# Kernel tuning notes

Hardware: AMD Instinct MI355X
Metric: run time of the kernel (lower is better)

The kernel has to match this reference:

```python
import jax, jax.numpy as jnp
import numpy as np
from jax import lax

NUM_INITS = 64
MODEL_MODE = ['conv', 'conv', 'dense']
SIZE_ARRAY = [(16, 1, 5, 5), (16,), (32, 16, 5, 5), (32,), (10, 512), (10,)]
_flat = [int(np.prod(s)) for s in SIZE_ARRAY]
BP = np.concatenate(([0], np.cumsum(_flat)))  # breakpoints into flat param vector
TOTAL_PARAMS = int(BP[-1])  # 18378
BATCH_N = 128


def setup_inputs() -> dict:
    key = jax.random.key(0)
    k1, k2 = jax.random.split(key)
    params = jax.random.normal(k1, (NUM_INITS, TOTAL_PARAMS), dtype=jnp.float32) * 0.05
    batch = jax.random.normal(k2, (BATCH_N, 1, 28, 28), dtype=jnp.float32)
    return {"params": params, "batch": batch}


def _conv_relu_pool(x, w, b):
    # x: (N, C_in, H, W), w: (C_out, C_in, k, k), b: (C_out,)
    y = lax.conv_general_dilated(x, w, window_strides=(1, 1), padding='VALID',
                                 dimension_numbers=('NCHW', 'OIHW', 'NCHW'))
    y = jax.nn.relu(y + b[None, :, None, None])
    # MaxPool2d(2, 2) over spatial dims
    return lax.reduce_window(y, -jnp.inf, lax.max, (1, 1, 2, 2), (1, 1, 2, 2), 'VALID')


def reference(params, batch):
    # out: (num_inits, N, C, H, W) — ensemble replicated batch
    out = jnp.broadcast_to(batch[None], (NUM_INITS,) + batch.shape)
    i = 0
    for mode in MODEL_MODE:
        w = params[:, BP[i]:BP[i + 1]].reshape((NUM_INITS,) + SIZE_ARRAY[i])
        b = params[:, BP[i + 1]:BP[i + 2]].reshape((NUM_INITS,) + SIZE_ARRAY[i + 1])
        if mode == 'conv':
            # grouped conv over inits == vmap of dense conv over the init axis
            out = jax.vmap(_conv_relu_pool)(out, w, b)
        else:  # dense
            out = out.reshape(out.shape[0], out.shape[1], -1)  # flatten C,H,W
            out = jnp.einsum('inf,iof->ino', out, w) + b[:, None, :]
        i += 2
    return jax.nn.log_softmax(out, axis=2)  # (num_inits, N, 10)
```

## Files before the change

### kernel.cpp

```cpp
#include <hip/hip_runtime.h>
#include <hip/hip_bf16.h>
#include <math.h>

#define P_TOTAL 18378

typedef __attribute__((ext_vector_type(8))) short short8;
typedef __attribute__((ext_vector_type(4))) float float4v;
typedef __attribute__((ext_vector_type(16))) float float16;

__device__ __forceinline__ unsigned short f2bf(float f) {
    union { float f; unsigned u; } v; v.f = f;
    unsigned r = v.u + 0x7fffu + ((v.u >> 16) & 1u);
    return (unsigned short)(r >> 16);
}
__device__ __forceinline__ float bf2f(unsigned short h) {
    union { unsigned u; float f; } v; v.u = ((unsigned)h) << 16;
    return v.f;
}

__global__ __launch_bounds__(256) void prep_kernel(
        const float* __restrict__ params,
        const float* __restrict__ batch,
        unsigned short* __restrict__ wswz,
        float* __restrict__ w3lf,
        unsigned short* __restrict__ w1bf,
        unsigned short* __restrict__ Bmat) {
    int blk = blockIdx.x;
    int t = threadIdx.x;
    if (blk < 64) {
        int i = blk;
        const float* w2 = params + (size_t)i * P_TOTAL + 416;
        unsigned short* dst = wswz + (size_t)i * 12800;
        for (int k = t; k < 12800; k += 256) {
            int co = k / 400;
            int r = k - co * 400;
            int cin = r / 25;
            int s = r - cin * 25;
            dst[(s * 32 + co) * 16 + cin] = f2bf(w2[k]);
        }
        const float* w3 = params + (size_t)i * P_TOTAL + 13248;
        float* d3 = w3lf + (size_t)i * 5120;
        for (int k = t; k < 5120; k += 256) {
            int o = k >> 9, r = k & 511;
            int l = r >> 3, s = r & 7;
            int co = l & 31, h = l >> 5;
            int py = s >> 1, d = s & 1;
            d3[k] = w3[o * 512 + co * 16 + py * 4 + 2 * h + d];
        }
        const float* w1 = params + (size_t)i * P_TOTAL;
        unsigned short* d1 = w1bf + (size_t)i * 512;
        for (int e = t; e < 512; e += 256) {
            int m = e >> 5, k = e & 31;
            d1[e] = (k < 25) ? f2bf(w1[m * 25 + k]) : (unsigned short)0;
        }
    } else {
        __shared__ float img[784];
        int j = blk - 64;
        const float* ip = batch + j * 784;
        for (int k = t; k < 784; k += 256) img[k] = ip[k];
        __syncthreads();
        unsigned short* dst = Bmat + (size_t)j * 18432;
        for (int task = t; task < 2304; task += 256) {
            int c = task >> 2, kh = task & 3;
            int pp = c >> 2, q = c & 3;
            int py = pp / 12, px = pp - py * 12;
            int y0 = 2 * py + (q >> 1);
            int x0 = 2 * px + (q & 1);
            unsigned short ov[8] __attribute__((aligned(16)));
#pragma unroll
            for (int u = 0; u < 8; ++u) {
                int k = kh * 8 + u;
                float v = 0.f;
                if (k < 25) {
                    int ky = k / 5, kx = k - ky * 5;
                    v = img[(y0 + ky) * 28 + x0 + kx];
                }
                ov[u] = f2bf(v);
            }
            *(uint4*)(dst + c * 32 + kh * 8) = *(const uint4*)ov;
        }
    }
}

#define A1_PIX_STRIDE 24
#define IMG_LDS (144 * A1_PIX_STRIDE)
__global__ __launch_bounds__(256, 5) void mega_kernel(
        const float* __restrict__ params,
        const unsigned short* __restrict__ Bmat,
        const unsigned short* __restrict__ w1bf,
        const unsigned short* __restrict__ wswz,
        const float* __restrict__ w3lf,
        float* __restrict__ out) {
    __shared__ unsigned short a1s[4 * IMG_LDS];
    int b = blockIdx.x;
    int i = b & 63;
    int g = b >> 6;
    int t = threadIdx.x;
    int w = t >> 6;
    int lane = t & 63;
    int j = g * 4 + w;

    {
        int co = lane & 15;
        int h4 = lane >> 4;
        short8 wfr = *(const short8*)(w1bf + (size_t)i * 512 + co * 32 + h4 * 8);
        float bias1 = params[(size_t)i * P_TOTAL + 400 + co];
        unsigned short* dst = a1s + w * IMG_LDS;
        const unsigned short* bsrc = Bmat + (size_t)j * 18432;
#pragma unroll 6
        for (int nt = 0; nt < 36; ++nt) {
            short8 afr = *(const short8*)(bsrc + (nt * 16 + co) * 32 + h4 * 8);
            float4v acc = {0.f, 0.f, 0.f, 0.f};
            acc = __builtin_amdgcn_mfma_f32_16x16x32_bf16(afr, wfr, acc, 0, 0, 0);
            float v = fmaxf(fmaxf(acc[0], acc[1]), fmaxf(acc[2], acc[3]));
            v = fmaxf(v + bias1, 0.f);
            dst[(nt * 4 + h4) * A1_PIX_STRIDE + co] = f2bf(v);
        }
    }

    int n = lane & 31;
    int h = lane >> 5;
    const short8* wg = (const short8*)(wswz + (size_t)i * 12800 + n * 16 + h * 8);
    int y0 = n >> 3, x0 = n & 7;
    const unsigned short* bbase = a1s + w * IMG_LDS;
    const short8* pptr0 = (const short8*)(bbase + ((y0    ) * 12 + x0) * A1_PIX_STRIDE + h * 8);
    const short8* pptr1 = (const short8*)(bbase + ((y0 + 4) * 12 + x0) * A1_PIX_STRIDE + h * 8);

    float16 acc0 = {};
    float16 acc1 = {};
#pragma unroll
    for (int ky = 0; ky < 5; ++ky) {
#pragma unroll
        for (int kx = 0; kx < 5; ++kx) {
            int tap = ky * 5 + kx;
            short8 wf = wg[tap * 64];
            int bo = (ky * 12 + kx) * 3;
            short8 p0 = pptr0[bo];
            short8 p1 = pptr1[bo];
            acc0 = __builtin_amdgcn_mfma_f32_32x32x16_bf16(p0, wf, acc0, 0, 0, 0);
            acc1 = __builtin_amdgcn_mfma_f32_32x32x16_bf16(p1, wf, acc1, 0, 0, 0);
        }
    }

    int co2 = lane & 31;
    float bias2 = params[(size_t)i * P_TOTAL + 13216 + co2];
    float xr[8];
#pragma unroll
    for (int pyl = 0; pyl < 2; ++pyl) {
#pragma unroll
        for (int d = 0; d < 2; ++d) {
            int base = pyl * 8 + d * 2;
            float v0 = fmaxf(fmaxf(acc0[base], acc0[base + 1]),
                             fmaxf(acc0[base + 4], acc0[base + 5]));
            float v1 = fmaxf(fmaxf(acc1[base], acc1[base + 1]),
                             fmaxf(acc1[base + 4], acc1[base + 5]));
            xr[pyl * 2 + d]     = fmaxf(v0 + bias2, 0.f);
            xr[4 + pyl * 2 + d] = fmaxf(v1 + bias2, 0.f);
        }
    }

    const float* w3p = w3lf + (size_t)i * 5120 + lane * 8;
    float acc[10];
#pragma unroll
    for (int o = 0; o < 10; ++o) {
        float4v u0 = *(const float4v*)(w3p + o * 512);
        float4v u1 = *(const float4v*)(w3p + o * 512 + 4);
        float a = 0.f;
        a = fmaf(xr[0], u0[0], a);
        a = fmaf(xr[1], u0[1], a);
        a = fmaf(xr[2], u0[2], a);
        a = fmaf(xr[3], u0[3], a);
        a = fmaf(xr[4], u1[0], a);
        a = fmaf(xr[5], u1[1], a);
        a = fmaf(xr[6], u1[2], a);
        a = fmaf(xr[7], u1[3], a);
#pragma unroll
        for (int d = 32; d >= 1; d >>= 1) a += __shfl_xor(a, d, 64);
        acc[o] = a;
    }
    const float* bp = params + (size_t)i * P_TOTAL + 18368;
    float m = -3.4e38f;
#pragma unroll
    for (int o = 0; o < 10; ++o) { acc[o] += bp[o]; m = fmaxf(m, acc[o]); }
    float ssum = 0.f;
#pragma unroll
    for (int o = 0; o < 10; ++o) ssum += __expf(acc[o] - m);
    float ls = __logf(ssum) + m;
    if (lane == 0) {
        float* op = out + ((size_t)i * 128 + j) * 10;
#pragma unroll
        for (int o = 0; o < 10; ++o) op[o] = acc[o] - ls;
    }
}

extern "C" void kernel_launch(void* const* d_in, const int* in_sizes, int n_in,
                              void* d_out, int out_size, void* d_ws, size_t ws_size,
                              hipStream_t stream) {
    const float* params = (const float*)d_in[0];
    const float* batch  = (const float*)d_in[1];
    float* out = (float*)d_out;

    unsigned short* wswz = (unsigned short*)d_ws;
    float* w3lf = (float*)((char*)d_ws + 1638400);
    unsigned short* w1bf = (unsigned short*)((char*)d_ws + 1638400 + 1310720);
    unsigned short* Bmat = (unsigned short*)((char*)d_ws + 1638400 + 1310720 + 65536);

    prep_kernel<<<192, 256, 0, stream>>>(params, batch, wswz, w3lf, w1bf, Bmat);
    mega_kernel<<<2048, 256, 0, stream>>>(params, Bmat, w1bf, wswz, w3lf, out);
}
```

Before: 105.5 us.

## Split prep work across more blocks, use DPP reductions, hardware bf16 convert, setprio

The prep kernel now splits each init's weight reformatting across 8 blocks and each image's im2col across 2 blocks, giving 768 blocks instead of 192 so more of the GPU is used during the prep phase. In the main kernel, the 64-lane shuffle-xor reduction becomes a DPP row/bcast sequence that leaves the total in lane 63, and only that lane computes the log-softmax. The float-to-bf16 conversion now uses the v_cvt_pk_bf16_f32 instruction, and s_setprio raises wave priority around the MFMA loop. The DPP broadcast steps depend on exact lane semantics, so a wrong control code would give wrong sums.

```diff
diff --git a/kernel.cpp b/kernel.cpp
--- a/kernel.cpp
+++ b/kernel.cpp
@@ -9,13 +9,23 @@
 typedef __attribute__((ext_vector_type(16))) float float16;
 
 __device__ __forceinline__ unsigned short f2bf(float f) {
-    union { float f; unsigned u; } v; v.f = f;
-    unsigned r = v.u + 0x7fffu + ((v.u >> 16) & 1u);
-    return (unsigned short)(r >> 16);
-}
-__device__ __forceinline__ float bf2f(unsigned short h) {
-    union { unsigned u; float f; } v; v.u = ((unsigned)h) << 16;
-    return v.f;
+    unsigned r;
+    asm("v_cvt_pk_bf16_f32 %0, %1, %1" : "=v"(r) : "v"(f));
+    return (unsigned short)r;
+}
+
+#define DPP_ADD_STEP(x, ctrl)                                                  \
+    x += __int_as_float(__builtin_amdgcn_update_dpp(                           \
+            0, __float_as_int(x), ctrl, 0xf, 0xf, true))
+
+__device__ __forceinline__ float wave_reduce_sum63(float x) {
+    DPP_ADD_STEP(x, 0x111);
+    DPP_ADD_STEP(x, 0x112);
+    DPP_ADD_STEP(x, 0x114);
+    DPP_ADD_STEP(x, 0x118);
+    DPP_ADD_STEP(x, 0x142);
+    DPP_ADD_STEP(x, 0x143);
+    return x;
 }
 
 __global__ __launch_bounds__(256) void prep_kernel(
@@ -27,40 +37,45 @@
         unsigned short* __restrict__ Bmat) {
     int blk = blockIdx.x;
     int t = threadIdx.x;
-    if (blk < 64) {
-        int i = blk;
-        const float* w2 = params + (size_t)i * P_TOTAL + 416;
-        unsigned short* dst = wswz + (size_t)i * 12800;
-        for (int k = t; k < 12800; k += 256) {
-            int co = k / 400;
-            int r = k - co * 400;
-            int cin = r / 25;
-            int s = r - cin * 25;
-            dst[(s * 32 + co) * 16 + cin] = f2bf(w2[k]);
-        }
-        const float* w3 = params + (size_t)i * P_TOTAL + 13248;
-        float* d3 = w3lf + (size_t)i * 5120;
-        for (int k = t; k < 5120; k += 256) {
-            int o = k >> 9, r = k & 511;
-            int l = r >> 3, s = r & 7;
-            int co = l & 31, h = l >> 5;
-            int py = s >> 1, d = s & 1;
-            d3[k] = w3[o * 512 + co * 16 + py * 4 + 2 * h + d];
-        }
-        const float* w1 = params + (size_t)i * P_TOTAL;
-        unsigned short* d1 = w1bf + (size_t)i * 512;
-        for (int e = t; e < 512; e += 256) {
-            int m = e >> 5, k = e & 31;
-            d1[e] = (k < 25) ? f2bf(w1[m * 25 + k]) : (unsigned short)0;
+    if (blk < 512) {
+        int i = blk >> 3;
+        int p = blk & 7;
+        const float* P = params + (size_t)i * P_TOTAL;
+        int s0 = p * 2304;
+        for (int s = s0 + t; s < s0 + 2304; s += 256) {
+            if (s < 12800) {
+                int co = s / 400;
+                int r = s - co * 400;
+                int cin = r / 25;
+                int sk = r - cin * 25;
+                wswz[(size_t)i * 12800 + (sk * 32 + co) * 16 + cin] =
+                    f2bf(P[416 + s]);
+            } else if (s < 17920) {
+                int k = s - 12800;
+                int o = k >> 9, r = k & 511;
+                int l = r >> 3, sl = r & 7;
+                int co = l & 31, h = l >> 5;
+                int py = sl >> 1, d = sl & 1;
+                w3lf[(size_t)i * 5120 + k] =
+                    P[13248 + o * 512 + co * 16 + py * 4 + 2 * h + d];
+            } else {
+                int e = s - 17920;
+                int m = e >> 5, k = e & 31;
+                w1bf[(size_t)i * 512 + e] =
+                    (k < 25) ? f2bf(P[m * 25 + k]) : (unsigned short)0;
+            }
         }
     } else {
         __shared__ float img[784];
-        int j = blk - 64;
+        int jb = blk - 512;
+        int j = jb >> 1;
+        int half = jb & 1;
         const float* ip = batch + j * 784;
         for (int k = t; k < 784; k += 256) img[k] = ip[k];
         __syncthreads();
         unsigned short* dst = Bmat + (size_t)j * 18432;
-        for (int task = t; task < 2304; task += 256) {
+        int task0 = half * 1152;
+        for (int task = task0 + t; task < task0 + 1152; task += 256) {
             int c = task >> 2, kh = task & 3;
             int pp = c >> 2, q = c & 3;
             int py = pp / 12, px = pp - py * 12;
@@ -128,6 +143,7 @@
 
     float16 acc0 = {};
     float16 acc1 = {};
+    __builtin_amdgcn_s_setprio(1);
 #pragma unroll
     for (int ky = 0; ky < 5; ++ky) {
 #pragma unroll
@@ -141,6 +157,7 @@
             acc1 = __builtin_amdgcn_mfma_f32_32x32x16_bf16(p1, wf, acc1, 0, 0, 0);
         }
     }
+    __builtin_amdgcn_s_setprio(0);
 
     int co2 = lane & 31;
     float bias2 = params[(size_t)i * P_TOTAL + 13216 + co2];
@@ -174,19 +191,17 @@
         a = fmaf(xr[5], u1[1], a);
         a = fmaf(xr[6], u1[2], a);
         a = fmaf(xr[7], u1[3], a);
-#pragma unroll
-        for (int d = 32; d >= 1; d >>= 1) a += __shfl_xor(a, d, 64);
-        acc[o] = a;
-    }
-    const float* bp = params + (size_t)i * P_TOTAL + 18368;
-    float m = -3.4e38f;
-#pragma unroll
-    for (int o = 0; o < 10; ++o) { acc[o] += bp[o]; m = fmaxf(m, acc[o]); }
-    float ssum = 0.f;
-#pragma unroll
-    for (int o = 0; o < 10; ++o) ssum += __expf(acc[o] - m);
-    float ls = __logf(ssum) + m;
-    if (lane == 0) {
+        acc[o] = wave_reduce_sum63(a);
+    }
+    if (lane == 63) {
+        const float* bp = params + (size_t)i * P_TOTAL + 18368;
+        float m = -3.4e38f;
+#pragma unroll
+        for (int o = 0; o < 10; ++o) { acc[o] += bp[o]; m = fmaxf(m, acc[o]); }
+        float ssum = 0.f;
+#pragma unroll
+        for (int o = 0; o < 10; ++o) ssum += __expf(acc[o] - m);
+        float ls = __logf(ssum) + m;
         float* op = out + ((size_t)i * 128 + j) * 10;
 #pragma unroll
         for (int o = 0; o < 10; ++o) op[o] = acc[o] - ls;
@@ -205,6 +220,6 @@
     unsigned short* w1bf = (unsigned short*)((char*)d_ws + 1638400 + 1310720);
     unsigned short* Bmat = (unsigned short*)((char*)d_ws + 1638400 + 1310720 + 65536);
 
-    prep_kernel<<<192, 256, 0, stream>>>(params, batch, wswz, w3lf, w1bf, Bmat);
+    prep_kernel<<<768, 256, 0, stream>>>(params, batch, wswz, w3lf, w1bf, Bmat);
     mega_kernel<<<2048, 256, 0, stream>>>(params, Bmat, w1bf, wswz, w3lf, out);
 }
```

After: 97.50 us. 1.08x faster.
